# Optimization experiments

Measured on AMD Instinct MI355X. Metric: run time of the kernel, lower is better.

The kernel has to match this reference:

```python
import jax, jax.numpy as jnp
import numpy as np

RANK = 32
ALPHA = 1.0
SCALE = ALPHA / RANK


def setup_inputs() -> dict:
    key = jax.random.key(0)
    k1, k2, k3, k4, k5 = jax.random.split(key, 5)
    B_, S, D_in, D_out = 4, 2048, 4096, 4096
    x = jax.random.normal(k1, (B_, S, D_in), dtype=jnp.float32)
    # nn.Linear weight: [out, in], kaiming-ish scale
    W = jax.random.normal(k2, (D_out, D_in), dtype=jnp.float32) / np.sqrt(D_in)
    bias = jax.random.normal(k3, (D_out,), dtype=jnp.float32) * 0.01
    A = jax.random.normal(k4, (D_in, RANK), dtype=jnp.float32) * 0.01
    # torch init is zeros for B; use small random so output depends on LoRA path
    Bm = jax.random.normal(k5, (RANK, D_out), dtype=jnp.float32) * 0.01
    return {"x": x, "W": W, "bias": bias, "A": A, "B": Bm}


def reference(x, W, bias, A, B):
    # Original: y = x @ (W + scale*(A@B)^T)^T + bias
    # Mathematically identical fused form (two GEMMs, no [in,out] delta):
    base = jnp.einsum('bsd,od->bso', x, W)          # [B,S,out]
    lora = jnp.einsum('bsr,ro->bso', x @ A, B)       # [B,S,rank]->[B,S,out]
    return base + SCALE * lora + bias
```

## Files before the change

kernel.cpp:

```cpp
#include <hip/hip_runtime.h>
#include <hip/hip_bf16.h>
#include <stdint.h>

#define RANK 32
#define SCALE (1.0f / 32.0f)

typedef __bf16 bf16x8 __attribute__((ext_vector_type(8)));
typedef float f32x4 __attribute__((ext_vector_type(4)));

__device__ __forceinline__ void gload16(const void* g, void* l) {
  __builtin_amdgcn_global_load_lds(
      (const __attribute__((address_space(1))) unsigned int*)g,
      (__attribute__((address_space(3))) unsigned int*)l, 16, 0, 0);
}

__device__ __forceinline__ unsigned short f2bf(float f) {
  __hip_bfloat16 h = __float2bfloat16(f);
  return *reinterpret_cast<unsigned short*>(&h);
}

__global__ __launch_bounds__(256) void transpose_B_k(const float* __restrict__ B,
                                                     float* __restrict__ Bt,
                                                     int Dout) {
  int idx = blockIdx.x * 256 + threadIdx.x;
  int r = idx / Dout;
  int o = idx - r * Dout;
  Bt[(long long)o * RANK + r] = B[idx];
}

__global__ __launch_bounds__(256) void merge_W_k(const float* __restrict__ W,
                                                 const float* __restrict__ A,
                                                 const float* __restrict__ Bt,
                                                 unsigned short* __restrict__ Wb,
                                                 int Din, int Dout) {
  __shared__ float sB[16 * RANK];
  int nib = Din / 256;
  int ib = blockIdx.x % nib;
  int ob = blockIdx.x / nib;
  int i0 = ib * 256, o0 = ob * 16;
  int t = threadIdx.x;

  if (t < 128) {
    reinterpret_cast<float4*>(sB)[t] =
        reinterpret_cast<const float4*>(Bt + (long long)o0 * RANK)[t];
  }

  float a[RANK];
  const float4* Ap = reinterpret_cast<const float4*>(A + (long long)(i0 + t) * RANK);
#pragma unroll
  for (int c = 0; c < RANK / 4; ++c) {
    float4 v = Ap[c];
    a[c * 4 + 0] = v.x; a[c * 4 + 1] = v.y;
    a[c * 4 + 2] = v.z; a[c * 4 + 3] = v.w;
  }
  __syncthreads();

  for (int o = 0; o < 16; ++o) {
    float d = 0.f;
#pragma unroll
    for (int j = 0; j < RANK; ++j) d += a[j] * sB[o * RANK + j];
    long long off = (long long)(o0 + o) * Din + i0 + t;
    float w = __builtin_nontemporal_load(&W[off]);
    Wb[off] = f2bf(w + SCALE * d);
  }
}

__global__ __launch_bounds__(256) void cast_x_k(const float* __restrict__ in,
                                                unsigned short* __restrict__ out,
                                                long long n8) {
  long long i = (long long)blockIdx.x * 256 + threadIdx.x;
  if (i >= n8) return;
  const f32x4* in4 = reinterpret_cast<const f32x4*>(in) + i * 2;
  f32x4 v0 = __builtin_nontemporal_load(in4);
  f32x4 v1 = __builtin_nontemporal_load(in4 + 1);
  union { unsigned short u[8]; uint4 q; } p;
  p.u[0] = f2bf(v0.x); p.u[1] = f2bf(v0.y); p.u[2] = f2bf(v0.z); p.u[3] = f2bf(v0.w);
  p.u[4] = f2bf(v1.x); p.u[5] = f2bf(v1.y); p.u[6] = f2bf(v1.z); p.u[7] = f2bf(v1.w);
  reinterpret_cast<uint4*>(out)[i] = p.q;
}

__device__ __forceinline__ void stage1(const unsigned short* g, int K, int koff,
                                       int row0, unsigned short* ldsbase,
                                       int t, int wid) {
  int r = t >> 2;
  int cg = (t & 3) ^ ((r ^ (r >> 2)) & 3);
  gload16(g + (long long)(row0 + r) * K + koff + cg * 8,
          ldsbase + row0 * 32 + wid * 512);
}

__device__ __forceinline__ int swz_off32(int rowl, int k) {
  return rowl * 32 + ((((k) >> 3) ^ ((rowl ^ (rowl >> 2)) & 3)) << 3);
}

__global__ __launch_bounds__(512, 2) void gemm256_bias_k(
    const unsigned short* __restrict__ Xb,
    const unsigned short* __restrict__ Wb,
    const float* __restrict__ bias,
    float* __restrict__ Out,
    int M, int N, int K) {
  __shared__ unsigned short As[2][256 * 32];
  __shared__ unsigned short Bs[2][256 * 32];

  int nbn = N / 256;
  int cpx = gridDim.x >> 3;
  int bid = blockIdx.x;
  int xcd = bid & 7, local = bid >> 3;
  int bm, bn;
  int mrows = cpx / nbn;
  if (mrows * nbn == cpx) {
    bn = local / mrows;
    bm = xcd * mrows + (local - bn * mrows);
  } else {
    int swz = xcd * cpx + local;
    bm = swz / nbn; bn = swz % nbn;
  }

  int t = threadIdx.x;
  int wid = t >> 6, lane = t & 63;
  int wr = wid >> 2, wc = wid & 3;
  int lr = lane & 15, kq = (lane >> 4) * 8;
  int wr64 = wr * 64, wc32 = wc * 32;

  const unsigned short* ga = Xb + (long long)bm * 256 * K;
  const unsigned short* gb = Wb + (long long)bn * 256 * K;

  f32x4 acc[8][4] = {};
  bf16x8 aL0[4], aL1[4], aH0[4], aH1[4], bF0[4], bF1[4];

#define LDA(BUF, ROWBASE) \
  (*(const bf16x8*)&As[BUF][swz_off32((ROWBASE) + lr, kq)])
#define LDB(BUF, ROWBASE) \
  (*(const bf16x8*)&Bs[BUF][swz_off32((ROWBASE) + lr, kq)])

#define GATE(NSTR) \
  asm volatile("s_waitcnt vmcnt(" NSTR ")" ::: "memory"); \
  __builtin_amdgcn_s_barrier();

#define READ_AH(AH, BUF) \
  AH[0] = LDA(BUF, 128 + wr64);      AH[1] = LDA(BUF, 128 + wr64 + 16); \
  AH[2] = LDA(BUF, 128 + wr64 + 32); AH[3] = LDA(BUF, 128 + wr64 + 48);

#define READ_LOB(AL, BF, BUF) \
  AL[0] = LDA(BUF, wr64);      AL[1] = LDA(BUF, wr64 + 16); \
  AL[2] = LDA(BUF, wr64 + 32); AL[3] = LDA(BUF, wr64 + 48); \
  BF[0] = LDB(BUF, wc32);            BF[1] = LDB(BUF, wc32 + 16); \
  BF[2] = LDB(BUF, 128 + wc32);      BF[3] = LDB(BUF, 128 + wc32 + 16);

#define MFMA16(AF, BF, MO)                                                   \
  __builtin_amdgcn_sched_barrier(0);                                         \
  __builtin_amdgcn_s_setprio(1);                                             \
  _Pragma("unroll")                                                          \
  for (int m = 0; m < 4; ++m)                                                \
    _Pragma("unroll")                                                        \
    for (int n = 0; n < 4; ++n)                                              \
      acc[(MO) + m][n] = __builtin_amdgcn_mfma_f32_16x16x32_bf16(            \
          AF[m], BF[n], acc[(MO) + m][n], 0, 0, 0);                          \
  __builtin_amdgcn_s_setprio(0);

  stage1(ga, K, 0, 0,    &As[0][0], t, wid);
  stage1(gb, K, 0, 0,    &Bs[0][0], t, wid);
  stage1(gb, K, 0, 128,  &Bs[0][0], t, wid);
  stage1(ga, K, 0, 128,  &As[0][0], t, wid);
  stage1(ga, K, 32, 0,   &As[1][0], t, wid);
  stage1(gb, K, 32, 0,   &Bs[1][0], t, wid);
  stage1(gb, K, 32, 128, &Bs[1][0], t, wid);
  asm volatile("s_waitcnt vmcnt(4)" ::: "memory");
  __builtin_amdgcn_s_barrier();
  READ_LOB(aL0, bF0, 0)

  for (int j = 0; j < 63; ++j) {
    int ko = j * 64;
    GATE("3")
    stage1(ga, K, ko + 32, 128, &As[1][0], t, wid);
    READ_AH(aH0, 0)
    MFMA16(aL0, bF0, 0)
    GATE("1")
    stage1(ga, K, ko + 64, 0,   &As[0][0], t, wid);
    stage1(gb, K, ko + 64, 0,   &Bs[0][0], t, wid);
    stage1(gb, K, ko + 64, 128, &Bs[0][0], t, wid);
    READ_LOB(aL1, bF1, 1)
    MFMA16(aH0, bF0, 4)
    GATE("3")
    stage1(ga, K, ko + 64, 128, &As[0][0], t, wid);
    READ_AH(aH1, 1)
    MFMA16(aL1, bF1, 0)
    GATE("1")
    stage1(ga, K, ko + 96, 0,   &As[1][0], t, wid);
    stage1(gb, K, ko + 96, 0,   &Bs[1][0], t, wid);
    stage1(gb, K, ko + 96, 128, &Bs[1][0], t, wid);
    READ_LOB(aL0, bF0, 0)
    MFMA16(aH1, bF1, 4)
  }

  GATE("3")
  stage1(ga, K, 127 * 32, 128, &As[1][0], t, wid);
  READ_AH(aH0, 0)
  MFMA16(aL0, bF0, 0)
  GATE("1")
  READ_LOB(aL1, bF1, 1)
  MFMA16(aH0, bF0, 4)
  GATE("0")
  READ_AH(aH1, 1)
  MFMA16(aL1, bF1, 0)
  MFMA16(aH1, bF1, 4)

#undef LDA
#undef LDB
#undef GATE
#undef READ_AH
#undef READ_LOB
#undef MFMA16

  int rq = (lane >> 4) * 4;
#pragma unroll
  for (int n = 0; n < 4; ++n) {
    int gc = bn * 256 + (n >= 2 ? 128 : 0) + wc32 + (n & 1) * 16 + lr;
    float bv = bias[gc];
#pragma unroll
    for (int m = 0; m < 8; ++m) {
      long long gr = (long long)bm * 256 + (m >= 4 ? 128 : 0) + wr64 + (m & 3) * 16 + rq;
#pragma unroll
      for (int v = 0; v < 4; ++v)
        __builtin_nontemporal_store(acc[m][n][v] + bv, &Out[(gr + v) * N + gc]);
    }
  }
}

extern "C" void kernel_launch(void* const* d_in, const int* in_sizes, int n_in,
                              void* d_out, int out_size, void* d_ws, size_t ws_size,
                              hipStream_t stream) {
  const float* x    = (const float*)d_in[0];
  const float* W    = (const float*)d_in[1];
  const float* bias = (const float*)d_in[2];
  const float* A    = (const float*)d_in[3];
  const float* B    = (const float*)d_in[4];

  int Din  = in_sizes[3] / RANK;
  int Dout = in_sizes[4] / RANK;
  long long M = (long long)in_sizes[0] / Din;

  size_t xb_bytes = (size_t)M * Din * 2;
  size_t wb_bytes = (size_t)Dout * Din * 2;
  size_t bt_bytes = (size_t)Dout * RANK * 4;
  if (ws_size < xb_bytes + wb_bytes + bt_bytes) return;

  char* ws = (char*)d_ws;
  unsigned short* Xb = (unsigned short*)ws;
  unsigned short* Wb = (unsigned short*)(ws + xb_bytes);
  float* Bt          = (float*)(ws + xb_bytes + wb_bytes);

  transpose_B_k<<<dim3((Dout * RANK) / 256), dim3(256), 0, stream>>>(B, Bt, Dout);
  merge_W_k<<<dim3((Dout / 16) * (Din / 256)), dim3(256), 0, stream>>>(W, A, Bt, Wb, Din, Dout);
  long long n8 = M * Din / 8;
  cast_x_k<<<dim3((unsigned)(n8 / 256)), dim3(256), 0, stream>>>(x, Xb, n8);
  gemm256_bias_k<<<dim3((unsigned)((M / 256) * (Dout / 256))), dim3(512), 0, stream>>>(
      Xb, Wb, bias, (float*)d_out, (int)M, Dout, Din);
}
```

Measured before the change: 345.8 us.

## Pre-pack merged weight into MFMA fragment layout and load B directly to registers

The merge kernel now writes the bf16 merged weight in a layout where each 16x32 MFMA B-fragment is 512 contiguous elements indexed by lane. The GEMM then drops the B shared-memory tiles and loads B fragments straight from global memory into registers, with the waitcnt gates rearranged for the new load counts. This removes LDS traffic, LDS capacity and bank pressure for B. In exchange, each wave loads its own B fragments, so waves sharing a column duplicate those global/L2 reads that LDS used to share, and global latency now sits directly before the MFMAs.

```diff
diff --git a/kernel.cpp b/kernel.cpp
--- a/kernel.cpp
+++ b/kernel.cpp
@@ -31,7 +31,7 @@
 __global__ __launch_bounds__(256) void merge_W_k(const float* __restrict__ W,
                                                  const float* __restrict__ A,
                                                  const float* __restrict__ Bt,
-                                                 unsigned short* __restrict__ Wb,
+                                                 unsigned short* __restrict__ Wbf,
                                                  int Din, int Dout) {
   __shared__ float sB[16 * RANK];
   int nib = Din / 256;
@@ -55,13 +55,19 @@
   }
   __syncthreads();
 
+  int i = i0 + t;
+  int KB = Din / 32;
+  long long fragrow = (long long)(o0 >> 4) * KB + (i >> 5);
+  int slot_base = ((i & 31) >> 3) * 16;
+  int e = i & 7;
+
   for (int o = 0; o < 16; ++o) {
     float d = 0.f;
 #pragma unroll
     for (int j = 0; j < RANK; ++j) d += a[j] * sB[o * RANK + j];
-    long long off = (long long)(o0 + o) * Din + i0 + t;
+    long long off = (long long)(o0 + o) * Din + i;
     float w = __builtin_nontemporal_load(&W[off]);
-    Wb[off] = f2bf(w + SCALE * d);
+    Wbf[fragrow * 512 + (slot_base + o) * 8 + e] = f2bf(w + SCALE * d);
   }
 }
 
@@ -94,12 +100,11 @@
 
 __global__ __launch_bounds__(512, 2) void gemm256_bias_k(
     const unsigned short* __restrict__ Xb,
-    const unsigned short* __restrict__ Wb,
+    const unsigned short* __restrict__ Wbf,
     const float* __restrict__ bias,
     float* __restrict__ Out,
     int M, int N, int K) {
   __shared__ unsigned short As[2][256 * 32];
-  __shared__ unsigned short Bs[2][256 * 32];
 
   int nbn = N / 256;
   int cpx = gridDim.x >> 3;
@@ -122,15 +127,15 @@
   int wr64 = wr * 64, wc32 = wc * 32;
 
   const unsigned short* ga = Xb + (long long)bm * 256 * K;
-  const unsigned short* gb = Wb + (long long)bn * 256 * K;
+  const int KB = K / 32;
+  const unsigned short* gbf = Wbf + ((long long)(bn * 16 + wc * 2) * KB) * 512
+                                  + lane * 8;
 
   f32x4 acc[8][4] = {};
-  bf16x8 aL0[4], aL1[4], aH0[4], aH1[4], bF0[4], bF1[4];
+  bf16x8 aL0[4], aL1[4], aH0[4], aH1[4], Bv0[4], Bv1[4];
 
 #define LDA(BUF, ROWBASE) \
   (*(const bf16x8*)&As[BUF][swz_off32((ROWBASE) + lr, kq)])
-#define LDB(BUF, ROWBASE) \
-  (*(const bf16x8*)&Bs[BUF][swz_off32((ROWBASE) + lr, kq)])
 
 #define GATE(NSTR) \
   asm volatile("s_waitcnt vmcnt(" NSTR ")" ::: "memory"); \
@@ -140,11 +145,16 @@
   AH[0] = LDA(BUF, 128 + wr64);      AH[1] = LDA(BUF, 128 + wr64 + 16); \
   AH[2] = LDA(BUF, 128 + wr64 + 32); AH[3] = LDA(BUF, 128 + wr64 + 48);
 
-#define READ_LOB(AL, BF, BUF) \
+#define READ_AL(AL, BUF) \
   AL[0] = LDA(BUF, wr64);      AL[1] = LDA(BUF, wr64 + 16); \
-  AL[2] = LDA(BUF, wr64 + 32); AL[3] = LDA(BUF, wr64 + 48); \
-  BF[0] = LDB(BUF, wc32);            BF[1] = LDB(BUF, wc32 + 16); \
-  BF[2] = LDB(BUF, 128 + wc32);      BF[3] = LDB(BUF, 128 + wc32 + 16);
+  AL[2] = LDA(BUF, wr64 + 32); AL[3] = LDA(BUF, wr64 + 48);
+
+#define LOADB(BV, T) { \
+  const unsigned short* fb = gbf + (long long)(T) * 512;               \
+  BV[0] = *(const bf16x8*)(fb);                                        \
+  BV[1] = *(const bf16x8*)(fb + (long long)KB * 512);                  \
+  BV[2] = *(const bf16x8*)(fb + (long long)8 * KB * 512);              \
+  BV[3] = *(const bf16x8*)(fb + (long long)9 * KB * 512); }
 
 #define MFMA16(AF, BF, MO)                                                   \
   __builtin_amdgcn_sched_barrier(0);                                         \
@@ -158,57 +168,53 @@
   __builtin_amdgcn_s_setprio(0);
 
   stage1(ga, K, 0, 0,    &As[0][0], t, wid);
-  stage1(gb, K, 0, 0,    &Bs[0][0], t, wid);
-  stage1(gb, K, 0, 128,  &Bs[0][0], t, wid);
   stage1(ga, K, 0, 128,  &As[0][0], t, wid);
+  LOADB(Bv0, 0)
   stage1(ga, K, 32, 0,   &As[1][0], t, wid);
-  stage1(gb, K, 32, 0,   &Bs[1][0], t, wid);
-  stage1(gb, K, 32, 128, &Bs[1][0], t, wid);
-  asm volatile("s_waitcnt vmcnt(4)" ::: "memory");
+  asm volatile("s_waitcnt vmcnt(1)" ::: "memory");
   __builtin_amdgcn_s_barrier();
-  READ_LOB(aL0, bF0, 0)
+  READ_AL(aL0, 0)
 
   for (int j = 0; j < 63; ++j) {
     int ko = j * 64;
-    GATE("3")
+    GATE("1")
     stage1(ga, K, ko + 32, 128, &As[1][0], t, wid);
+    LOADB(Bv1, 2 * j + 1)
     READ_AH(aH0, 0)
-    MFMA16(aL0, bF0, 0)
+    MFMA16(aL0, Bv0, 0)
+    GATE("5")
+    stage1(ga, K, ko + 64, 0, &As[0][0], t, wid);
+    READ_AL(aL1, 1)
+    MFMA16(aH0, Bv0, 4)
     GATE("1")
-    stage1(ga, K, ko + 64, 0,   &As[0][0], t, wid);
-    stage1(gb, K, ko + 64, 0,   &Bs[0][0], t, wid);
-    stage1(gb, K, ko + 64, 128, &Bs[0][0], t, wid);
-    READ_LOB(aL1, bF1, 1)
-    MFMA16(aH0, bF0, 4)
-    GATE("3")
     stage1(ga, K, ko + 64, 128, &As[0][0], t, wid);
+    LOADB(Bv0, 2 * j + 2)
     READ_AH(aH1, 1)
-    MFMA16(aL1, bF1, 0)
-    GATE("1")
-    stage1(ga, K, ko + 96, 0,   &As[1][0], t, wid);
-    stage1(gb, K, ko + 96, 0,   &Bs[1][0], t, wid);
-    stage1(gb, K, ko + 96, 128, &Bs[1][0], t, wid);
-    READ_LOB(aL0, bF0, 0)
-    MFMA16(aH1, bF1, 4)
-  }
-
-  GATE("3")
+    MFMA16(aL1, Bv1, 0)
+    GATE("5")
+    stage1(ga, K, ko + 96, 0, &As[1][0], t, wid);
+    READ_AL(aL0, 0)
+    MFMA16(aH1, Bv1, 4)
+  }
+
+  GATE("1")
   stage1(ga, K, 127 * 32, 128, &As[1][0], t, wid);
+  LOADB(Bv1, 127)
   READ_AH(aH0, 0)
-  MFMA16(aL0, bF0, 0)
-  GATE("1")
-  READ_LOB(aL1, bF1, 1)
-  MFMA16(aH0, bF0, 4)
+  MFMA16(aL0, Bv0, 0)
+  GATE("5")
+  READ_AL(aL1, 1)
+  MFMA16(aH0, Bv0, 4)
   GATE("0")
   READ_AH(aH1, 1)
-  MFMA16(aL1, bF1, 0)
-  MFMA16(aH1, bF1, 4)
+  MFMA16(aL1, Bv1, 0)
+  MFMA16(aH1, Bv1, 4)
 
 #undef LDA
-#undef LDB
 #undef GATE
 #undef READ_AH
-#undef READ_LOB
+#undef READ_AL
+#undef LOADB
 #undef MFMA16
 
   int rq = (lane >> 4) * 4;
@@ -245,14 +251,14 @@
   if (ws_size < xb_bytes + wb_bytes + bt_bytes) return;
 
   char* ws = (char*)d_ws;
-  unsigned short* Xb = (unsigned short*)ws;
-  unsigned short* Wb = (unsigned short*)(ws + xb_bytes);
-  float* Bt          = (float*)(ws + xb_bytes + wb_bytes);
+  unsigned short* Xb  = (unsigned short*)ws;
+  unsigned short* Wbf = (unsigned short*)(ws + xb_bytes);
+  float* Bt           = (float*)(ws + xb_bytes + wb_bytes);
 
   transpose_B_k<<<dim3((Dout * RANK) / 256), dim3(256), 0, stream>>>(B, Bt, Dout);
-  merge_W_k<<<dim3((Dout / 16) * (Din / 256)), dim3(256), 0, stream>>>(W, A, Bt, Wb, Din, Dout);
+  merge_W_k<<<dim3((Dout / 16) * (Din / 256)), dim3(256), 0, stream>>>(W, A, Bt, Wbf, Din, Dout);
   long long n8 = M * Din / 8;
   cast_x_k<<<dim3((unsigned)(n8 / 256)), dim3(256), 0, stream>>>(x, Xb, n8);
   gemm256_bias_k<<<dim3((unsigned)((M / 256) * (Dout / 256))), dim3(512), 0, stream>>>(
-      Xb, Wb, bias, (float*)d_out, (int)M, Dout, Din);
-}
+      Xb, Wbf, bias, (float*)d_out, (int)M, Dout, Din);
+}
```

New measurement: 329.5 us. 1.05x faster.
